# Kernel tuning notes

Measured on AMD Instinct MI355X. Metric: run time of the kernel, lower is better.

## Reference

```python
import jax, jax.numpy as jnp
import numpy as np

EPS = 1e-7
N_SAMPLES = 8   # matches n_samples init kwarg
W_ITERS = 64    # fixed-trip-count replacement for the data-dependent rejection loop


def _sample_w(key, kappa, m_int):
    # Wood (1994) rejection sampler for the radial component w, vectorized
    # over all elements with a fixed number of iterations (no host sync).
    m = jnp.asarray(float(m_int), kappa.dtype)
    s = jnp.sqrt(4.0 * kappa ** 2 + m ** 2)
    b = (-2.0 * kappa + s) / m
    a = (m + 2.0 * kappa + s) / 4.0
    d = 4.0 * a * b / (1.0 + b) - m * jnp.log(m)
    shape = kappa.shape

    def body(carry, it):
        w, done = carry
        k = jax.random.fold_in(key, it)
        k_eps, k_u = jax.random.split(k)
        eps = jnp.clip(jax.random.uniform(k_eps, shape, kappa.dtype), EPS, 1.0 - EPS)
        u = jax.random.uniform(k_u, shape, kappa.dtype)
        denom = 1.0 - (1.0 - b) * eps
        cos_theta = (1.0 - (1.0 + b) * eps) / denom
        t = 2.0 * a * b / denom
        accept = (m * jnp.log(t) - t + d >= jnp.log(u)) & (~done)
        return (jnp.where(accept, cos_theta, w), done | accept), None

    init = (jnp.zeros(shape, kappa.dtype), jnp.zeros(shape, bool))
    (w, done), _ = jax.lax.scan(body, init, jnp.arange(W_ITERS))
    return jnp.where(done, w, jnp.ones_like(w))


def _vmf_rsample(key, mu, kappa, n_samples):
    # mu: (..., D) unit vectors; kappa: (...,). Returns (n_samples, ..., D).
    batch_shape = mu.shape[:-1]
    D = mu.shape[-1]
    exp_shape = (n_samples,) + batch_shape
    k_w, k_v = jax.random.split(key)
    kappa_e = jnp.broadcast_to(kappa, exp_shape)
    w = _sample_w(k_w, kappa_e, D - 1)                       # (S, ...)
    v = jax.random.normal(k_v, exp_shape + (D - 1,), mu.dtype)
    v = v / jnp.linalg.norm(v, axis=-1, keepdims=True)
    w_sq = jnp.clip(1.0 - w ** 2, EPS, None)
    z = jnp.concatenate([w[..., None], jnp.sqrt(w_sq)[..., None] * v], axis=-1)
    # Householder rotation mapping e1 -> mu
    e1 = jnp.zeros_like(mu).at[..., 0].set(1.0)
    u = e1 - mu
    u = u / jnp.clip(jnp.linalg.norm(u, axis=-1, keepdims=True), EPS, None)
    dot = jnp.sum(z * u, axis=-1, keepdims=True)
    return z - 2.0 * dot * u


def setup_inputs() -> dict:
    key = jax.random.key(0)
    ks = jax.random.split(key, 6)
    B, D, NNEG = 4096, 64, 128

    def unit(k, shape):
        x = jax.random.normal(k, shape, jnp.float32)
        return x / jnp.linalg.norm(x, axis=-1, keepdims=True)

    mu_ref = unit(ks[0], (B, D))
    mu_pos = unit(ks[1], (B, 1, D))
    mu_neg = unit(ks[2], (B, NNEG, D))
    kappa_ref = 10.0 + 30.0 * jax.random.uniform(ks[3], (B,), jnp.float32)
    kappa_pos = 10.0 + 30.0 * jax.random.uniform(ks[4], (B, 1), jnp.float32)
    kappa_neg = 10.0 + 30.0 * jax.random.uniform(ks[5], (B, NNEG), jnp.float32)
    loss_kappa = jnp.ones((1,), jnp.float32) * 16.0
    return {
        "mu_ref": mu_ref, "kappa_ref": kappa_ref,
        "mu_pos": mu_pos, "kappa_pos": kappa_pos,
        "mu_neg": mu_neg, "kappa_neg": kappa_neg,
        "loss_kappa": loss_kappa,
    }


def reference(mu_ref, kappa_ref, mu_pos, kappa_pos, mu_neg, kappa_neg, loss_kappa):
    key = jax.random.key(42)
    kr, kp, kn = jax.random.split(key, 3)
    mu_ref_e = mu_ref[:, None, :]          # (B,1,D)
    kappa_ref_e = kappa_ref[:, None]       # (B,1)
    s_ref = _vmf_rsample(kr, mu_ref_e, kappa_ref_e, N_SAMPLES)   # (S,B,1,D)
    s_pos = _vmf_rsample(kp, mu_pos, kappa_pos, N_SAMPLES)       # (S,B,1,D)
    s_neg = _vmf_rsample(kn, mu_neg, kappa_neg, N_SAMPLES)       # (S,B,n_neg,D)

    sim_pos = jnp.sum(s_ref * s_pos, axis=-1) * loss_kappa       # (S,B,1)
    sim_neg = jnp.sum(s_ref * s_neg, axis=-1) * loss_kappa       # (S,B,n_neg)

    neg_lse = jax.nn.logsumexp(sim_neg, axis=-1)                 # (S,B)
    sp = sim_pos[..., 0]                                         # (S,B)
    log_denom = jax.nn.logsumexp(jnp.stack([sp, neg_lse], axis=0), axis=0)
    log_prob = jax.nn.logsumexp(sp - log_denom, axis=0) - jnp.log(jnp.float32(N_SAMPLES))
    return -jnp.mean(log_prob)
```

## Files before the change

### kernel.cpp

```cpp
#include <hip/hip_runtime.h>
#include <stdint.h>


#define NB 4096
#define NNEG 128
#define DD 64
#define NS 8
#define NIT 64

#define LOG2E 1.4426950408889634f
#define LN2   0.6931471805599453f

__device__ __forceinline__ void tf2x32(uint32_t k0, uint32_t k1,
                                       uint32_t x0, uint32_t x1,
                                       uint32_t& y0, uint32_t& y1) {
  uint32_t ks2 = k0 ^ k1 ^ 0x1BD11BDAu;
  x0 += k0; x1 += k1;
#define TFR(r) { x0 += x1; x1 = __builtin_rotateleft32(x1, r); x1 ^= x0; }
  TFR(13) TFR(15) TFR(26) TFR(6)
  x0 += k1; x1 += ks2 + 1u;
  TFR(17) TFR(29) TFR(16) TFR(24)
  x0 += ks2; x1 += k0 + 2u;
  TFR(13) TFR(15) TFR(26) TFR(6)
  x0 += k0; x1 += k1 + 3u;
  TFR(17) TFR(29) TFR(16) TFR(24)
  x0 += k1; x1 += ks2 + 4u;
  TFR(13) TFR(15) TFR(26) TFR(6)
  x0 += ks2; x1 += k0 + 5u;
#undef TFR
  y0 = x0; y1 = x1;
}

__device__ __forceinline__ float u01f(uint32_t bits) {
  return __uint_as_float(0x3F800000u | (bits >> 9)) - 1.0f;
}

__device__ __forceinline__ float normal_from_bits(uint32_t bits) {
  float f = u01f(bits);
  float x = fmaf(f, 2.0f, -0.99999994f);
  float s = fmaf(-x, x, 1.0f);
  float w2 = __builtin_amdgcn_logf(s);
  float p;
  if (w2 > -7.2134752f) {
    float y = fmaf(w2, -0.69314718f, -2.5f);
    p =              3.9742602e-08f;
    p = fmaf(p, y,   4.8546266e-07f);
    p = fmaf(p, y,  -4.9828227e-06f);
    p = fmaf(p, y,  -6.2105281e-06f);
    p = fmaf(p, y,   3.0912003e-04f);
    p = fmaf(p, y,  -1.7730349e-03f);
    p = fmaf(p, y,  -5.9081340e-03f);
    p = fmaf(p, y,   0.34880266f);
    p = fmaf(p, y,   2.1233135f);
  } else {
    float y = __builtin_amdgcn_sqrtf(-0.69314718f * w2) - 3.0f;
    p =             -2.8314572e-04f;
    p = fmaf(p, y,   1.4276565e-04f);
    p = fmaf(p, y,   1.9082601e-03f);
    p = fmaf(p, y,  -5.1950123e-03f);
    p = fmaf(p, y,   8.1168897e-03f);
    p = fmaf(p, y,  -1.0779792e-02f);
    p = fmaf(p, y,   1.3348578e-02f);
    p = fmaf(p, y,   1.4165811f);
    p = fmaf(p, y,   4.0064333f);
  }
  return p * x;
}

struct WPair { float lo, hi; };

__device__ __forceinline__ float wave_sum(float v) {
  for (int m = 32; m; m >>= 1) v += __shfl_xor(v, m, 64);
  return v;
}

__device__ __forceinline__ uint32_t hash32(uint32_t x) {
  x *= 0x9E3779B9u;
  x ^= x >> 16; x *= 0x21f0aaadu;
  x ^= x >> 15; x *= 0x735a2d97u;
  x ^= x >> 15;
  return x;
}

__device__ __forceinline__ float2 bm_pair(uint32_t bits) {
  float u1 = (float)((bits & 0xffffu) + 1u) * (1.0f / 65536.0f);
  float u2 = (float)(bits >> 16) * (1.0f / 65536.0f);
  float r  = __builtin_amdgcn_sqrtf(-2.0f * LN2 * __builtin_amdgcn_logf(u1));
  return {r * __builtin_amdgcn_cosf(u2), r * __builtin_amdgcn_sinf(u2)};
}
__device__ __forceinline__ float bm_one(uint32_t bits) {
  float u1 = (float)((bits & 0xffffu) + 1u) * (1.0f / 65536.0f);
  float u2 = (float)(bits >> 16) * (1.0f / 65536.0f);
  float r  = __builtin_amdgcn_sqrtf(-2.0f * LN2 * __builtin_amdgcn_logf(u1));
  return r * __builtin_amdgcn_cosf(u2);
}

__device__ WPair w_pair_shared(float kappa, uint32_t L) {
  float s   = __builtin_amdgcn_sqrtf(fmaf(4.0f * kappa, kappa, 3969.0f));
  float bb  = (s - 2.0f * kappa) * (1.0f / 63.0f);
  float aa  = (63.0f + 2.0f * kappa + s) * 0.25f;
  float ab2 = 2.0f * aa * bb;
  float dc  = 2.0f * ab2 * __builtin_amdgcn_rcpf(1.0f + bb) - 261.01749f;
  const float K = 43.668274f;
  float C   = fmaf(K, __builtin_amdgcn_logf(ab2), dc);
  float om_b = 1.0f - bb, op_b = 1.0f + bb;
  uint32_t base = 0x40000000u + (L << 6);
  float w0 = 1.0f, w1 = 1.0f;
  int k = 0;
  for (int it = 0; it < NIT; ++it) {
    if (__all(k >= 2)) break;
    uint32_t bits = hash32(base + (uint32_t)it);
    float eps = fmaxf((float)(bits & 0xffffu) * (1.0f / 65536.0f), 1e-7f);
    float uu  = (float)((bits >> 16) + 1u) * (1.0f / 65536.0f);
    float den = fmaf(-om_b, eps, 1.0f);
    float id  = __builtin_amdgcn_rcpf(den);
    float ct  = fmaf(-op_b, eps, 1.0f) * id;
    float tv  = ab2 * id;
    float lhs = fmaf(-K, __builtin_amdgcn_logf(den), C) - tv;
    bool acc = (lhs >= LN2 * __builtin_amdgcn_logf(uu)) && (k < 2);
    if (acc) {
      if (k == 0) w0 = ct; else w1 = ct;
      ++k;
    }
  }
  return {w0, w1};
}

__global__ __launch_bounds__(512) void refpos_wave(
    const float* __restrict__ mu_ref, const float* __restrict__ kap_ref,
    const float* __restrict__ mu_pos, const float* __restrict__ kap_pos,
    float* __restrict__ s_ref, float* __restrict__ s_pos) {
  __shared__ uint4 ktS[2][64];
  __shared__ uint2 kvS[2];
  int t = threadIdx.x;

  if (t < 128) {
    int g = t >> 6, it = t & 63;
    uint32_t gk0, gk1;
    if (g == 0) {
      uint32_t A0, B0, A1, B1;
      tf2x32(0u, 42u, 0u, 3u, A0, B0);
      tf2x32(0u, 42u, 1u, 4u, A1, B1);
      gk0 = A0; gk1 = A1;
    } else {
      uint32_t A2, B2, A0, B0;
      tf2x32(0u, 42u, 2u, 5u, A2, B2);
      tf2x32(0u, 42u, 0u, 3u, A0, B0);
      gk0 = A2; gk1 = B0;
    }
    uint32_t C0, D0, C1, D1;
    tf2x32(gk0, gk1, 0u, 2u, C0, D0);
    tf2x32(gk0, gk1, 1u, 3u, C1, D1);
    uint32_t E0, E1;
    tf2x32(C0, C1, 0u, (uint32_t)it, E0, E1);
    uint32_t F0, G0, F1, G1;
    tf2x32(E0, E1, 0u, 2u, F0, G0);
    tf2x32(E0, E1, 1u, 3u, F1, G1);
    ktS[g][it] = {F0, F1, G0, G1};
    if (it == 0) kvS[g] = {D0, D1};
  }
  __syncthreads();

  int wave_id = blockIdx.x * 8 + (t >> 6);
  int lane = t & 63;
  int g = wave_id >> 14;
  int r = wave_id & 16383;
  int b = r & 4095;
  const float* mu = (g == 0 ? mu_ref : mu_pos) + (size_t)b * DD;
  float kap = (g == 0 ? kap_ref[b] : kap_pos[b]);

  float s   = __builtin_amdgcn_sqrtf(fmaf(4.0f * kap, kap, 3969.0f));
  float bbv = (s - 2.0f * kap) * (1.0f / 63.0f);
  float aav = (63.0f + 2.0f * kap + s) * 0.25f;
  float ab2 = 2.0f * aav * bbv;
  float dcv = 2.0f * ab2 * __builtin_amdgcn_rcpf(1.0f + bbv) - 261.01749f;
  const float K = 43.668274f;
  float C   = fmaf(K, __builtin_amdgcn_logf(ab2), dcv);
  float om_b = 1.0f - bbv, op_b = 1.0f + bbv;

  uint4 kk = ktS[g][lane];
  uint32_t e0, e1, g0, g1;
  tf2x32(kk.x, kk.y, (uint32_t)r, (uint32_t)r + 16384u, e0, e1);
  tf2x32(kk.z, kk.w, (uint32_t)r, (uint32_t)r + 16384u, g0, g1);
  float ct0, ct1;
  bool acc0, acc1;
  {
    float eps = fminf(fmaxf(u01f(e0), 1e-7f), 0.99999988f);
    float den = fmaf(-om_b, eps, 1.0f);
    float id  = __builtin_amdgcn_rcpf(den);
    ct0 = fmaf(-op_b, eps, 1.0f) * id;
    float tv  = ab2 * id;
    float lhs = fmaf(-K, __builtin_amdgcn_logf(den), C) - tv;
    acc0 = lhs >= LN2 * __builtin_amdgcn_logf(u01f(g0));
  }
  {
    float eps = fminf(fmaxf(u01f(e1), 1e-7f), 0.99999988f);
    float den = fmaf(-om_b, eps, 1.0f);
    float id  = __builtin_amdgcn_rcpf(den);
    ct1 = fmaf(-op_b, eps, 1.0f) * id;
    float tv  = ab2 * id;
    float lhs = fmaf(-K, __builtin_amdgcn_logf(den), C) - tv;
    acc1 = lhs >= LN2 * __builtin_amdgcn_logf(u01f(g1));
  }
  unsigned long long m0 = __ballot(acc0);
  unsigned long long m1 = __ballot(acc1);
  int f0i = __ffsll((long long)m0);
  int f1i = __ffsll((long long)m1);
  float w0 = f0i ? __shfl(ct0, f0i - 1, 64) : 1.0f;
  float w1 = f1i ? __shfl(ct1, f1i - 1, 64) : 1.0f;

  uint2 kv = kvS[g];
  float v0 = 0.f, v1 = 0.f, m1v = 0.f;
  if (lane < 63) {
    uint32_t Lv = (uint32_t)r * 63u + (uint32_t)lane;
    uint32_t y0, y1;
    tf2x32(kv.x, kv.y, Lv, Lv + 1032192u, y0, y1);
    v0 = normal_from_bits(y0);
    v1 = normal_from_bits(y1);
    m1v = mu[lane + 1];
  }
  float mu0 = mu[0];
  float ss0 = wave_sum(v0 * v0);
  float ss1 = wave_sum(v1 * v1);
  float mv0 = wave_sum(m1v * v0);
  float mv1 = wave_sum(m1v * v1);
  float msq = wave_sum(m1v * m1v);

  float c0 = __builtin_amdgcn_sqrtf(fmaxf(1.0f - w0 * w0, 1e-7f));
  float c1 = __builtin_amdgcn_sqrtf(fmaxf(1.0f - w1 * w1, 1e-7f));
  float e0m = 1.0f - mu0;
  float nu  = fmaxf(__builtin_amdgcn_sqrtf(e0m * e0m + msq), 1e-7f);
  float inu = __builtin_amdgcn_rcpf(nu);
  float f0 = c0 * __builtin_amdgcn_rsqf(ss0);
  float f1 = c1 * __builtin_amdgcn_rsqf(ss1);
  float dot0 = (w0 * e0m - f0 * mv0) * inu;
  float dot1 = (w1 * e0m - f1 * mv1) * inu;

  float* outp = (g == 0 ? s_ref : s_pos);
  float* row0 = outp + (size_t)r * DD;
  float* row1 = outp + (size_t)(r + 16384) * DD;
  if (lane < 63) {
    float uh = -m1v * inu;
    row0[lane + 1] = f0 * v0 - 2.0f * dot0 * uh;
    row1[lane + 1] = f1 * v1 - 2.0f * dot1 * uh;
  } else {
    row0[0] = w0 - 2.0f * dot0 * (e0m * inu);
    row1[0] = w1 - 2.0f * dot1 * (e0m * inu);
  }
}

__global__ __launch_bounds__(512, 4) void neg_kernel(
    const float* __restrict__ mu_neg, const float* __restrict__ kap_neg,
    const float* __restrict__ s_ref, const float* __restrict__ s_pos,
    const float* __restrict__ loss_kappa, float* __restrict__ t_out) {
  __shared__ float4 muS4[128 * 17];
  __shared__ float4 rx4[4][16];
  __shared__ float4 ry4[4][16];
  __shared__ float posS[8][64];
  __shared__ float rrS[8];
  __shared__ float wreds[8][2];
  int b = blockIdx.x;
  int t = threadIdx.x;
  int n = t >> 7;
  int j = t & 127;
  int lane = t & 63;
  int wid = t >> 6;

  const float4* mublk4 = (const float4*)(mu_neg + (size_t)b * (NNEG * DD));
  for (int i = t; i < NNEG * 16; i += 512)
    muS4[(i >> 4) * 17 + (i & 15)] = mublk4[i];
  {
    int h = wid >> 2, nn = wid & 3;
    size_t row = (size_t)(nn * 4096 + b) + (size_t)h * 16384;
    float rv = s_ref[row * DD + lane];
    float* dst = (h == 0) ? (float*)&rx4[nn][0] : (float*)&ry4[nn][0];
    dst[lane] = rv;
    posS[wid][lane] = s_pos[row * DD + lane];
    float nrsq = wave_sum(lane > 0 ? rv * rv : 0.0f);
    if (lane == 0) rrS[wid] = nrsq;
  }
  __syncthreads();

  int blk = n * 4096 + b;
  float kap = kap_neg[(size_t)b * NNEG + j];
  uint32_t L = (uint32_t)blk * 128u + (uint32_t)j;
  WPair wp = w_pair_shared(kap, L);

  const float4* myMu4 = &muS4[j * 17];
  const float4* rxp = rx4[n];
  const float4* ryp = ry4[n];
  float fd0 = 0.f, fd1 = 0.f;
#pragma unroll 2
  for (int c = 0; c < 16; ++c) {
    float4 m4 = myMu4[c];
    float4 rx = rxp[c];
    float4 ry = ryp[c];
    fd0 = fmaf(m4.x, rx.x, fd0); fd0 = fmaf(m4.y, rx.y, fd0);
    fd0 = fmaf(m4.z, rx.z, fd0); fd0 = fmaf(m4.w, rx.w, fd0);
    fd1 = fmaf(m4.x, ry.x, fd1); fd1 = fmaf(m4.y, ry.y, fd1);
    fd1 = fmaf(m4.z, ry.z, fd1); fd1 = fmaf(m4.w, ry.w, fd1);
  }
  float mu0 = ((const float*)myMu4)[0];
  float rf0 = ((const float*)rxp)[0];
  float rf1 = ((const float*)ryp)[0];
  float rm0 = fd0 - rf0 * mu0;
  float rm1 = fd1 - rf1 * mu0;
  float msq = fmaxf(fmaf(-mu0, mu0, 1.0f), 0.0f);
  float lk  = loss_kappa[0];
  float e0m = 1.0f - mu0;
  float nu  = fmaxf(__builtin_amdgcn_sqrtf(e0m + e0m), 1e-7f);
  float inu = __builtin_amdgcn_rcpf(nu);

  auto simf = [&](float wv, float rm, float rfv, float rr, uint32_t cnt) {
    float2 ab = bm_pair(hash32(cnt + 15u));
    float x3 = bm_one(hash32(cnt));
    float th = fmaf(0.060358835f, x3, 0.99635702f);
    float s61 = 61.0f * th * th * th;
    float ss  = fmaf(ab.x, ab.x, fmaf(ab.y, ab.y, s61));
    float nr  = fmaxf(__builtin_amdgcn_sqrtf(rr), 1e-6f);
    float pp  = rm * __builtin_amdgcn_rcpf(nr);
    float qq  = __builtin_amdgcn_sqrtf(fmaxf(msq - pp * pp, 0.0f));
    float rv  = nr * ab.x;
    float mv  = fmaf(pp, ab.x, qq * ab.y);
    float c   = __builtin_amdgcn_sqrtf(fmaxf(1.0f - wv * wv, 1e-7f));
    float f   = c * __builtin_amdgcn_rsqf(ss);
    float dd  = (wv * e0m - f * mv) * inu;
    float rz  = rfv * wv + f * rv;
    float ru  = (rfv * e0m - rm) * inu;
    return lk * (rz - 2.0f * dd * ru);
  };
  float sim0 = simf(wp.lo, rm0, rf0, rrS[n],     L << 4);
  float sim1 = simf(wp.hi, rm1, rf1, rrS[4 + n], (2097152u + L) << 4);

  float z0 = wave_sum(__builtin_amdgcn_exp2f(sim0 * LOG2E));
  float z1 = wave_sum(__builtin_amdgcn_exp2f(sim1 * LOG2E));
  if (lane == 0) { wreds[wid][0] = z0; wreds[wid][1] = z1; }
  __syncthreads();
  float lse0 = LN2 * __builtin_amdgcn_logf(wreds[n*2][0] + wreds[n*2+1][0]);
  float lse1 = LN2 * __builtin_amdgcn_logf(wreds[n*2][1] + wreds[n*2+1][1]);

  if (j < 64) {
    float rxl = ((const float*)rxp)[lane];
    float ryl = ((const float*)ryp)[lane];
    float sp0 = wave_sum(rxl * posS[n][lane]) * lk;
    float sp1 = wave_sum(ryl * posS[4 + n][lane]) * lk;
    if (lane == 0) {
      float m0  = fmaxf(sp0, lse0);
      float ld0 = m0 + LN2 * __builtin_amdgcn_logf(
          __builtin_amdgcn_exp2f((sp0 - m0) * LOG2E) +
          __builtin_amdgcn_exp2f((lse0 - m0) * LOG2E));
      t_out[blk] = sp0 - ld0;
      float m1  = fmaxf(sp1, lse1);
      float ld1 = m1 + LN2 * __builtin_amdgcn_logf(
          __builtin_amdgcn_exp2f((sp1 - m1) * LOG2E) +
          __builtin_amdgcn_exp2f((lse1 - m1) * LOG2E));
      t_out[blk + 16384] = sp1 - ld1;
    }
  }
}

__global__ __launch_bounds__(256) void final_kernel(
    const float* __restrict__ t_tab, float* __restrict__ out) {
  __shared__ float red[256];
  int t = threadIdx.x;
  float acc = 0.f;
  for (int b = t; b < NB; b += 256) {
    float mx = -INFINITY;
    for (int n = 0; n < NS; ++n) mx = fmaxf(mx, t_tab[n * NB + b]);
    float s = 0.f;
    for (int n = 0; n < NS; ++n)
      s += __builtin_amdgcn_exp2f((t_tab[n * NB + b] - mx) * LOG2E);
    acc += mx + LN2 * __builtin_amdgcn_logf(s) - 2.0794415f;
  }
  red[t] = acc; __syncthreads();
  for (int s = 128; s > 0; s >>= 1) {
    if (t < s) red[t] += red[t + s];
    __syncthreads();
  }
  if (t == 0) out[0] = -(red[0] / (float)NB);
}

extern "C" void kernel_launch(void* const* d_in, const int* in_sizes, int n_in,
                              void* d_out, int out_size, void* d_ws, size_t ws_size,
                              hipStream_t stream) {
  const float* mu_ref  = (const float*)d_in[0];
  const float* kap_ref = (const float*)d_in[1];
  const float* mu_pos  = (const float*)d_in[2];
  const float* kap_pos = (const float*)d_in[3];
  const float* mu_neg  = (const float*)d_in[4];
  const float* kap_neg = (const float*)d_in[5];
  const float* lk      = (const float*)d_in[6];
  float* out = (float*)d_out;

  uint8_t* ws = (uint8_t*)d_ws;
  float* s_ref = (float*)ws;
  float* s_pos = (float*)(ws + 8388608);
  float* t_tab = (float*)(ws + 2 * 8388608);

  refpos_wave<<<4096, 512, 0, stream>>>(mu_ref, kap_ref, mu_pos, kap_pos,
                                        s_ref, s_pos);
  neg_kernel<<<NB, 512, 0, stream>>>(mu_neg, kap_neg,
                                     s_ref, s_pos, lk, t_tab);
  final_kernel<<<1, 256, 0, stream>>>(t_tab, out);
}
```

Before: 97.36 us.

## Fuse ref/pos vMF sampling into the negative-similarity kernel

The ref and pos sample generation now runs inside the per-batch neg kernel, with each block computing its own 8 ref/pos rows directly into shared memory. This removes one kernel launch and the 16 MB write-then-read round trip of s_ref and s_pos through global workspace. The positive similarity is now computed from register-held pos samples. The launch bound is raised to 8 waves per SIMD target, which may constrain registers and cause spills in the larger fused kernel.

```diff
diff --git a/kernel.cpp b/kernel.cpp
--- a/kernel.cpp
+++ b/kernel.cpp
@@ -126,13 +126,26 @@
   return {w0, w1};
 }
 
-__global__ __launch_bounds__(512) void refpos_wave(
+__global__ __launch_bounds__(512, 8) void fused_kernel(
     const float* __restrict__ mu_ref, const float* __restrict__ kap_ref,
     const float* __restrict__ mu_pos, const float* __restrict__ kap_pos,
-    float* __restrict__ s_ref, float* __restrict__ s_pos) {
+    const float* __restrict__ mu_neg, const float* __restrict__ kap_neg,
+    const float* __restrict__ loss_kappa, float* __restrict__ t_out) {
+  __shared__ float4 muS4[128 * 17];
+  __shared__ float4 rx4[4][16];
+  __shared__ float4 ry4[4][16];
   __shared__ uint4 ktS[2][64];
   __shared__ uint2 kvS[2];
+  __shared__ float rrS[8];
+  __shared__ float wreds[8][2];
+  int b = blockIdx.x;
   int t = threadIdx.x;
+  int lane = t & 63;
+  int wid = t >> 6;
+
+  const float4* mublk4 = (const float4*)(mu_neg + (size_t)b * (NNEG * DD));
+  for (int i = t; i < NNEG * 16; i += 512)
+    muS4[(i >> 4) * 17 + (i & 15)] = mublk4[i];
 
   if (t < 128) {
     int g = t >> 6, it = t & 63;
@@ -161,126 +174,103 @@
   }
   __syncthreads();
 
-  int wave_id = blockIdx.x * 8 + (t >> 6);
-  int lane = t & 63;
-  int g = wave_id >> 14;
-  int r = wave_id & 16383;
-  int b = r & 4095;
-  const float* mu = (g == 0 ? mu_ref : mu_pos) + (size_t)b * DD;
-  float kap = (g == 0 ? kap_ref[b] : kap_pos[b]);
-
-  float s   = __builtin_amdgcn_sqrtf(fmaf(4.0f * kap, kap, 3969.0f));
-  float bbv = (s - 2.0f * kap) * (1.0f / 63.0f);
-  float aav = (63.0f + 2.0f * kap + s) * 0.25f;
-  float ab2 = 2.0f * aav * bbv;
-  float dcv = 2.0f * ab2 * __builtin_amdgcn_rcpf(1.0f + bbv) - 261.01749f;
-  const float K = 43.668274f;
-  float C   = fmaf(K, __builtin_amdgcn_logf(ab2), dcv);
-  float om_b = 1.0f - bbv, op_b = 1.0f + bbv;
-
-  uint4 kk = ktS[g][lane];
-  uint32_t e0, e1, g0, g1;
-  tf2x32(kk.x, kk.y, (uint32_t)r, (uint32_t)r + 16384u, e0, e1);
-  tf2x32(kk.z, kk.w, (uint32_t)r, (uint32_t)r + 16384u, g0, g1);
-  float ct0, ct1;
-  bool acc0, acc1;
+  float pv0, pv1;
+  int   elem;
   {
-    float eps = fminf(fmaxf(u01f(e0), 1e-7f), 0.99999988f);
-    float den = fmaf(-om_b, eps, 1.0f);
-    float id  = __builtin_amdgcn_rcpf(den);
-    ct0 = fmaf(-op_b, eps, 1.0f) * id;
-    float tv  = ab2 * id;
-    float lhs = fmaf(-K, __builtin_amdgcn_logf(den), C) - tv;
-    acc0 = lhs >= LN2 * __builtin_amdgcn_logf(u01f(g0));
-  }
-  {
-    float eps = fminf(fmaxf(u01f(e1), 1e-7f), 0.99999988f);
-    float den = fmaf(-om_b, eps, 1.0f);
-    float id  = __builtin_amdgcn_rcpf(den);
-    ct1 = fmaf(-op_b, eps, 1.0f) * id;
-    float tv  = ab2 * id;
-    float lhs = fmaf(-K, __builtin_amdgcn_logf(den), C) - tv;
-    acc1 = lhs >= LN2 * __builtin_amdgcn_logf(u01f(g1));
-  }
-  unsigned long long m0 = __ballot(acc0);
-  unsigned long long m1 = __ballot(acc1);
-  int f0i = __ffsll((long long)m0);
-  int f1i = __ffsll((long long)m1);
-  float w0 = f0i ? __shfl(ct0, f0i - 1, 64) : 1.0f;
-  float w1 = f1i ? __shfl(ct1, f1i - 1, 64) : 1.0f;
-
-  uint2 kv = kvS[g];
-  float v0 = 0.f, v1 = 0.f, m1v = 0.f;
-  if (lane < 63) {
-    uint32_t Lv = (uint32_t)r * 63u + (uint32_t)lane;
-    uint32_t y0, y1;
-    tf2x32(kv.x, kv.y, Lv, Lv + 1032192u, y0, y1);
-    v0 = normal_from_bits(y0);
-    v1 = normal_from_bits(y1);
-    m1v = mu[lane + 1];
-  }
-  float mu0 = mu[0];
-  float ss0 = wave_sum(v0 * v0);
-  float ss1 = wave_sum(v1 * v1);
-  float mv0 = wave_sum(m1v * v0);
-  float mv1 = wave_sum(m1v * v1);
-  float msq = wave_sum(m1v * m1v);
-
-  float c0 = __builtin_amdgcn_sqrtf(fmaxf(1.0f - w0 * w0, 1e-7f));
-  float c1 = __builtin_amdgcn_sqrtf(fmaxf(1.0f - w1 * w1, 1e-7f));
-  float e0m = 1.0f - mu0;
-  float nu  = fmaxf(__builtin_amdgcn_sqrtf(e0m * e0m + msq), 1e-7f);
-  float inu = __builtin_amdgcn_rcpf(nu);
-  float f0 = c0 * __builtin_amdgcn_rsqf(ss0);
-  float f1 = c1 * __builtin_amdgcn_rsqf(ss1);
-  float dot0 = (w0 * e0m - f0 * mv0) * inu;
-  float dot1 = (w1 * e0m - f1 * mv1) * inu;
-
-  float* outp = (g == 0 ? s_ref : s_pos);
-  float* row0 = outp + (size_t)r * DD;
-  float* row1 = outp + (size_t)(r + 16384) * DD;
-  if (lane < 63) {
-    float uh = -m1v * inu;
-    row0[lane + 1] = f0 * v0 - 2.0f * dot0 * uh;
-    row1[lane + 1] = f1 * v1 - 2.0f * dot1 * uh;
-  } else {
-    row0[0] = w0 - 2.0f * dot0 * (e0m * inu);
-    row1[0] = w1 - 2.0f * dot1 * (e0m * inu);
-  }
-}
-
-__global__ __launch_bounds__(512, 4) void neg_kernel(
-    const float* __restrict__ mu_neg, const float* __restrict__ kap_neg,
-    const float* __restrict__ s_ref, const float* __restrict__ s_pos,
-    const float* __restrict__ loss_kappa, float* __restrict__ t_out) {
-  __shared__ float4 muS4[128 * 17];
-  __shared__ float4 rx4[4][16];
-  __shared__ float4 ry4[4][16];
-  __shared__ float posS[8][64];
-  __shared__ float rrS[8];
-  __shared__ float wreds[8][2];
-  int b = blockIdx.x;
-  int t = threadIdx.x;
+    int g = wid >> 2, nn = wid & 3;
+    int r = nn * 4096 + b;
+    const float* mu = (g == 0 ? mu_ref : mu_pos) + (size_t)b * DD;
+    float kap = (g == 0 ? kap_ref[b] : kap_pos[b]);
+
+    float s   = __builtin_amdgcn_sqrtf(fmaf(4.0f * kap, kap, 3969.0f));
+    float bbv = (s - 2.0f * kap) * (1.0f / 63.0f);
+    float aav = (63.0f + 2.0f * kap + s) * 0.25f;
+    float ab2 = 2.0f * aav * bbv;
+    float dcv = 2.0f * ab2 * __builtin_amdgcn_rcpf(1.0f + bbv) - 261.01749f;
+    const float K = 43.668274f;
+    float C   = fmaf(K, __builtin_amdgcn_logf(ab2), dcv);
+    float om_b = 1.0f - bbv, op_b = 1.0f + bbv;
+
+    uint4 kk = ktS[g][lane];
+    uint32_t e0, e1, g0, g1;
+    tf2x32(kk.x, kk.y, (uint32_t)r, (uint32_t)r + 16384u, e0, e1);
+    tf2x32(kk.z, kk.w, (uint32_t)r, (uint32_t)r + 16384u, g0, g1);
+    float ct0, ct1;
+    bool acc0, acc1;
+    {
+      float eps = fminf(fmaxf(u01f(e0), 1e-7f), 0.99999988f);
+      float den = fmaf(-om_b, eps, 1.0f);
+      float id  = __builtin_amdgcn_rcpf(den);
+      ct0 = fmaf(-op_b, eps, 1.0f) * id;
+      float tv  = ab2 * id;
+      float lhs = fmaf(-K, __builtin_amdgcn_logf(den), C) - tv;
+      acc0 = lhs >= LN2 * __builtin_amdgcn_logf(u01f(g0));
+    }
+    {
+      float eps = fminf(fmaxf(u01f(e1), 1e-7f), 0.99999988f);
+      float den = fmaf(-om_b, eps, 1.0f);
+      float id  = __builtin_amdgcn_rcpf(den);
+      ct1 = fmaf(-op_b, eps, 1.0f) * id;
+      float tv  = ab2 * id;
+      float lhs = fmaf(-K, __builtin_amdgcn_logf(den), C) - tv;
+      acc1 = lhs >= LN2 * __builtin_amdgcn_logf(u01f(g1));
+    }
+    unsigned long long m0 = __ballot(acc0);
+    unsigned long long m1 = __ballot(acc1);
+    int f0i = __ffsll((long long)m0);
+    int f1i = __ffsll((long long)m1);
+    float w0 = f0i ? __shfl(ct0, f0i - 1, 64) : 1.0f;
+    float w1 = f1i ? __shfl(ct1, f1i - 1, 64) : 1.0f;
+
+    uint2 kv = kvS[g];
+    float v0 = 0.f, v1 = 0.f, m1v = 0.f;
+    if (lane < 63) {
+      uint32_t Lv = (uint32_t)r * 63u + (uint32_t)lane;
+      uint32_t y0, y1;
+      tf2x32(kv.x, kv.y, Lv, Lv + 1032192u, y0, y1);
+      v0 = normal_from_bits(y0);
+      v1 = normal_from_bits(y1);
+      m1v = mu[lane + 1];
+    }
+    float mu0 = mu[0];
+    float ss0 = wave_sum(v0 * v0);
+    float ss1 = wave_sum(v1 * v1);
+    float mv0 = wave_sum(m1v * v0);
+    float mv1 = wave_sum(m1v * v1);
+    float msq = wave_sum(m1v * m1v);
+
+    float c0 = __builtin_amdgcn_sqrtf(fmaxf(1.0f - w0 * w0, 1e-7f));
+    float c1 = __builtin_amdgcn_sqrtf(fmaxf(1.0f - w1 * w1, 1e-7f));
+    float e0m = 1.0f - mu0;
+    float nu  = fmaxf(__builtin_amdgcn_sqrtf(e0m * e0m + msq), 1e-7f);
+    float inu = __builtin_amdgcn_rcpf(nu);
+    float f0 = c0 * __builtin_amdgcn_rsqf(ss0);
+    float f1 = c1 * __builtin_amdgcn_rsqf(ss1);
+    float dot0 = (w0 * e0m - f0 * mv0) * inu;
+    float dot1 = (w1 * e0m - f1 * mv1) * inu;
+
+    if (lane < 63) {
+      float uh = -m1v * inu;
+      pv0 = fmaf(-2.0f * dot0, uh, f0 * v0);
+      pv1 = fmaf(-2.0f * dot1, uh, f1 * v1);
+      elem = lane + 1;
+    } else {
+      pv0 = w0 - 2.0f * dot0 * (e0m * inu);
+      pv1 = w1 - 2.0f * dot1 * (e0m * inu);
+      elem = 0;
+    }
+    if (g == 0) {
+      ((float*)&rx4[nn][0])[elem] = pv0;
+      ((float*)&ry4[nn][0])[elem] = pv1;
+      float q0 = wave_sum(lane < 63 ? pv0 * pv0 : 0.0f);
+      float q1 = wave_sum(lane < 63 ? pv1 * pv1 : 0.0f);
+      if (lane == 0) { rrS[nn] = q0; rrS[4 + nn] = q1; }
+    }
+  }
+  __syncthreads();
+
   int n = t >> 7;
   int j = t & 127;
-  int lane = t & 63;
-  int wid = t >> 6;
-
-  const float4* mublk4 = (const float4*)(mu_neg + (size_t)b * (NNEG * DD));
-  for (int i = t; i < NNEG * 16; i += 512)
-    muS4[(i >> 4) * 17 + (i & 15)] = mublk4[i];
-  {
-    int h = wid >> 2, nn = wid & 3;
-    size_t row = (size_t)(nn * 4096 + b) + (size_t)h * 16384;
-    float rv = s_ref[row * DD + lane];
-    float* dst = (h == 0) ? (float*)&rx4[nn][0] : (float*)&ry4[nn][0];
-    dst[lane] = rv;
-    posS[wid][lane] = s_pos[row * DD + lane];
-    float nrsq = wave_sum(lane > 0 ? rv * rv : 0.0f);
-    if (lane == 0) rrS[wid] = nrsq;
-  }
-  __syncthreads();
-
   int blk = n * 4096 + b;
   float kap = kap_neg[(size_t)b * NNEG + j];
   uint32_t L = (uint32_t)blk * 128u + (uint32_t)j;
@@ -336,25 +326,26 @@
   float z1 = wave_sum(__builtin_amdgcn_exp2f(sim1 * LOG2E));
   if (lane == 0) { wreds[wid][0] = z0; wreds[wid][1] = z1; }
   __syncthreads();
-  float lse0 = LN2 * __builtin_amdgcn_logf(wreds[n*2][0] + wreds[n*2+1][0]);
-  float lse1 = LN2 * __builtin_amdgcn_logf(wreds[n*2][1] + wreds[n*2+1][1]);
-
-  if (j < 64) {
-    float rxl = ((const float*)rxp)[lane];
-    float ryl = ((const float*)ryp)[lane];
-    float sp0 = wave_sum(rxl * posS[n][lane]) * lk;
-    float sp1 = wave_sum(ryl * posS[4 + n][lane]) * lk;
+
+  if (wid >= 4) {
+    int nn = wid & 3;
+    const float* rx = (const float*)&rx4[nn][0];
+    const float* ry = (const float*)&ry4[nn][0];
+    float sp0 = wave_sum(rx[elem] * pv0) * lk;
+    float sp1 = wave_sum(ry[elem] * pv1) * lk;
     if (lane == 0) {
+      float lse0 = LN2 * __builtin_amdgcn_logf(wreds[nn*2][0] + wreds[nn*2+1][0]);
+      float lse1 = LN2 * __builtin_amdgcn_logf(wreds[nn*2][1] + wreds[nn*2+1][1]);
       float m0  = fmaxf(sp0, lse0);
       float ld0 = m0 + LN2 * __builtin_amdgcn_logf(
           __builtin_amdgcn_exp2f((sp0 - m0) * LOG2E) +
           __builtin_amdgcn_exp2f((lse0 - m0) * LOG2E));
-      t_out[blk] = sp0 - ld0;
+      t_out[nn * 4096 + b] = sp0 - ld0;
       float m1  = fmaxf(sp1, lse1);
       float ld1 = m1 + LN2 * __builtin_amdgcn_logf(
           __builtin_amdgcn_exp2f((sp1 - m1) * LOG2E) +
           __builtin_amdgcn_exp2f((lse1 - m1) * LOG2E));
-      t_out[blk + 16384] = sp1 - ld1;
+      t_out[nn * 4096 + b + 16384] = sp1 - ld1;
     }
   }
 }
@@ -392,14 +383,9 @@
   const float* lk      = (const float*)d_in[6];
   float* out = (float*)d_out;
 
-  uint8_t* ws = (uint8_t*)d_ws;
-  float* s_ref = (float*)ws;
-  float* s_pos = (float*)(ws + 8388608);
-  float* t_tab = (float*)(ws + 2 * 8388608);
-
-  refpos_wave<<<4096, 512, 0, stream>>>(mu_ref, kap_ref, mu_pos, kap_pos,
-                                        s_ref, s_pos);
-  neg_kernel<<<NB, 512, 0, stream>>>(mu_neg, kap_neg,
-                                     s_ref, s_pos, lk, t_tab);
+  float* t_tab = (float*)d_ws;
+
+  fused_kernel<<<NB, 512, 0, stream>>>(mu_ref, kap_ref, mu_pos, kap_pos,
+                                       mu_neg, kap_neg, lk, t_tab);
   final_kernel<<<1, 256, 0, stream>>>(t_tab, out);
 }
```

Result: faster. 88.56 us (-9.0%).
